# Optimization experiments

Measured on AMD Instinct MI355X. Metric: run time of the kernel, lower is better.

The kernel has to match this reference:

```python
import jax, jax.numpy as jnp
import numpy as np

SCALE = 1.0 / 16.0      # spatial scale: image coords -> feature-map coords (stride-16 backbone)
OUT = 7                 # roi_pool_outsize
RATIO = 2               # sampling_ratio
NUM_CLASSES = 21
HID = 1024
SCORE_THRESH = 0.05
NMS_THRESH = 0.5
DET = 100               # detections_per_img
MIN_SIZE = 0.01
LOG_MAX = float(np.log(1000.0 / 16.0))  # standard bbox decode dw/dh clamp


def _bilinear(feat, ys, xs):
    # feat [C,H,W]; ys [Py], xs [Px] -> [C,Py,Px] (torchvision roi_align interpolation, aligned=False)
    C, H, W = feat.shape
    vy = (ys > -1.0) & (ys < H)
    vx = (xs > -1.0) & (xs < W)
    y = jnp.clip(ys, 0.0, H - 1.0)
    x = jnp.clip(xs, 0.0, W - 1.0)
    y0 = jnp.floor(y).astype(jnp.int32)
    x0 = jnp.floor(x).astype(jnp.int32)
    y1 = jnp.minimum(y0 + 1, H - 1)
    x1 = jnp.minimum(x0 + 1, W - 1)
    ly = (y - y0)[:, None]
    lx = (x - x0)[None, :]
    f00 = feat[:, y0[:, None], x0[None, :]]
    f01 = feat[:, y0[:, None], x1[None, :]]
    f10 = feat[:, y1[:, None], x0[None, :]]
    f11 = feat[:, y1[:, None], x1[None, :]]
    val = (f00 * (1.0 - ly) * (1.0 - lx) + f01 * (1.0 - ly) * lx
           + f10 * ly * (1.0 - lx) + f11 * ly * lx)
    return val * (vy[:, None] & vx[None, :])


def _roi_align(features, boxes, bidx):
    # features [N,C,H,W], boxes [R,4] (image coords), bidx [R] -> [R,C,OUT,OUT]
    N, C, H, W = features.shape
    b = boxes * SCALE
    rw = jnp.maximum(b[:, 2] - b[:, 0], 1.0)
    rh = jnp.maximum(b[:, 3] - b[:, 1], 1.0)
    bw = rw / OUT
    bh = rh / OUT
    # per-bin sample offsets: (ph + (i+0.5)/ratio) for ph in [0,OUT), i in [0,RATIO)
    g = (jnp.arange(OUT, dtype=jnp.float32)[:, None]
         + (jnp.arange(RATIO, dtype=jnp.float32)[None, :] + 0.5) / RATIO).reshape(-1)  # [OUT*RATIO]
    ys = b[:, 1][:, None] + g[None, :] * bh[:, None]  # [R, OUT*RATIO]
    xs = b[:, 0][:, None] + g[None, :] * bw[:, None]
    vals = jax.vmap(lambda i, yr, xr: _bilinear(features[i], yr, xr))(bidx, ys, xs)  # [R,C,P,P]
    R = boxes.shape[0]
    return vals.reshape(R, C, OUT, RATIO, OUT, RATIO).mean(axis=(3, 5))


def _decode(deltas, props):
    # deltas [R,K,4], props [R,4]; weights (10,10,5,5) as in the module
    pw = props[:, 2] - props[:, 0]
    ph = props[:, 3] - props[:, 1]
    pcx = props[:, 0] + 0.5 * pw
    pcy = props[:, 1] + 0.5 * ph
    dx = deltas[..., 0] / 10.0
    dy = deltas[..., 1] / 10.0
    dw = jnp.minimum(deltas[..., 2] / 5.0, LOG_MAX)
    dh = jnp.minimum(deltas[..., 3] / 5.0, LOG_MAX)
    cx = dx * pw[:, None] + pcx[:, None]
    cy = dy * ph[:, None] + pcy[:, None]
    w = jnp.exp(dw) * pw[:, None]
    h = jnp.exp(dh) * ph[:, None]
    return jnp.stack([cx - 0.5 * w, cy - 0.5 * h, cx + 0.5 * w, cy + 0.5 * h], axis=-1)


def _per_image(scores, boxes, img):
    # scores [S,K], boxes [S,K,4]. Drop background class, flatten, filter, class-aware NMS, top-DET.
    S, K = scores.shape
    sc = scores[:, 1:].reshape(-1)                 # [M]
    bx = boxes[:, 1:, :].reshape(-1, 4)            # [M,4]
    lb = jnp.broadcast_to(jnp.arange(1, K, dtype=jnp.int32)[None, :], (S, K - 1)).reshape(-1)
    wv = bx[:, 2] - bx[:, 0]
    hv = bx[:, 3] - bx[:, 1]
    valid = (sc > SCORE_THRESH) & (wv >= MIN_SIZE) & (hv >= MIN_SIZE)
    live0 = jnp.where(valid, sc, -1.0)
    # batched_nms via per-class coordinate offsets
    nb = bx + (lb.astype(bx.dtype) * (img + 1.0))[:, None]
    areas = (nb[:, 2] - nb[:, 0]) * (nb[:, 3] - nb[:, 1])

    def step(live, _):
        i = jnp.argmax(live)
        s = live[i]
        b = nb[i]
        xx1 = jnp.maximum(b[0], nb[:, 0])
        yy1 = jnp.maximum(b[1], nb[:, 1])
        xx2 = jnp.minimum(b[2], nb[:, 2])
        yy2 = jnp.minimum(b[3], nb[:, 3])
        inter = jnp.maximum(xx2 - xx1, 0.0) * jnp.maximum(yy2 - yy1, 0.0)
        area_i = (b[2] - b[0]) * (b[3] - b[1])
        iou = inter / (area_i + areas - inter + 1e-9)
        live = jnp.where(iou > NMS_THRESH, -1.0, live)  # also suppresses i itself (iou=1)
        return live, (i, s)

    _, (idxs, svals) = jax.lax.scan(step, live0, None, length=DET)
    keep = svals > SCORE_THRESH
    out_boxes = jnp.where(keep[:, None], bx[idxs], 0.0)
    out_scores = jnp.where(keep, svals, 0.0)
    out_labels = jnp.where(keep, lb[idxs], 0)
    return out_boxes, out_scores, out_labels


def _forward(features, proposals, w1, b1, w2, b2, wc, bc, wb, bb, image_size):
    N, C, H, W = features.shape
    S = proposals.shape[1]
    props = proposals.reshape(-1, 4)
    bidx = jnp.repeat(jnp.arange(N), S)
    feats = _roi_align(features, props, bidx)          # [R,C,7,7]
    x = feats.reshape(N * S, -1)                       # [R, C*49]
    h = jax.nn.relu(x @ w1 + b1)
    h = jax.nn.relu(h @ w2 + b2)
    cls = h @ wc + bc                                  # [R,K]
    deltas = (h @ wb + bb).reshape(N * S, NUM_CLASSES, 4)
    scores = jax.nn.softmax(cls, axis=-1)
    boxes = _decode(deltas, props)                     # [R,K,4]
    img = float(image_size)
    boxes = jnp.clip(boxes, 0.0, img)                  # square image -> clip both coords to [0,img]
    scores = scores.reshape(N, S, NUM_CLASSES)
    boxes = boxes.reshape(N, S, NUM_CLASSES, 4)
    return jax.vmap(lambda s, bx: _per_image(s, bx, img))(scores, boxes)


def setup_inputs() -> dict:
    key = jax.random.key(0)
    ks = jax.random.split(key, 12)
    N, S, C, H, W = 2, 512, 512, 50, 50
    IMG = 800
    features = jax.random.normal(ks[0], (N, C, H, W), jnp.float32)
    x1 = jax.random.uniform(ks[1], (N, S)) * (IMG - 80.0)
    y1 = jax.random.uniform(ks[2], (N, S)) * (IMG - 80.0)
    x2 = jnp.minimum(x1 + 16.0 + jax.random.uniform(ks[3], (N, S)) * 180.0, float(IMG))
    y2 = jnp.minimum(y1 + 16.0 + jax.random.uniform(ks[4], (N, S)) * 180.0, float(IMG))
    proposals = jnp.stack([x1, y1, x2, y2], axis=-1)
    D = C * OUT * OUT  # 25088
    w1 = jax.random.normal(ks[5], (D, HID), jnp.float32) * 0.01
    b1 = jnp.zeros((HID,), jnp.float32)
    w2 = jax.random.normal(ks[6], (HID, HID), jnp.float32) * 0.02
    b2 = jnp.zeros((HID,), jnp.float32)
    wc = jax.random.normal(ks[7], (HID, NUM_CLASSES), jnp.float32) * 0.05
    bc = jnp.zeros((NUM_CLASSES,), jnp.float32)
    wb = jax.random.normal(ks[8], (HID, NUM_CLASSES * 4), jnp.float32) * 0.02
    bb = jnp.zeros((NUM_CLASSES * 4,), jnp.float32)
    return {"features": features, "proposals": proposals, "w1": w1, "b1": b1,
            "w2": w2, "b2": b2, "wc": wc, "bc": bc, "wb": wb, "bb": bb,
            "image_size": IMG}


def reference(features, proposals, w1, b1, w2, b2, wc, bc, wb, bb, image_size):
    boxes, scores, labels = _forward(features, proposals, w1, b1, w2, b2, wc, bc, wb, bb, image_size)
    return boxes, scores, labels
```

## Files before the change

### kernel.cpp

```cpp
#include <hip/hip_runtime.h>
#include <cmath>

#define NIMG 2
#define SPROP 512
#define NROI 1024
#define CCH 512
#define FH 50
#define FW 50
#define K1 25088
#define HID 1024
#define NCLS 21
#define NDET 100
#define IMGSZ 800.0f
#define LOGMAX 4.135166556742356f
#define MCAND 10240
#define ZSPLIT 8
#define KCHUNK 3136
#define ZSPLIT2 4
#define KCHUNK2 256

typedef unsigned short u16;
typedef __attribute__((ext_vector_type(8))) short short8;
typedef __attribute__((ext_vector_type(4))) float f32x4;
typedef __attribute__((ext_vector_type(16))) float f32x16;

__device__ __forceinline__ u16 f2bf(float x) {
  unsigned int u = __float_as_uint(x);
  u += 0x7fffu + ((u >> 16) & 1u);
  return (u16)(u >> 16);
}
__device__ __forceinline__ float bf2f(u16 h) {
  return __uint_as_float(((unsigned int)h) << 16);
}

template <bool BF16OUT>
__global__ __launch_bounds__(256) void roi_kernel(
    const float* __restrict__ feat, const float* __restrict__ props,
    float* __restrict__ X, u16* __restrict__ Xhi, u16* __restrict__ Xlo) {
  const int r = blockIdx.x;
  const int n = r >> 9;
  const int tid = threadIdx.x;
  __shared__ float tile[32][256];
  __shared__ int sy0[14], sy1[14], sx0[14], sx1[14];
  __shared__ float sly[14], slx[14], svy[14], svx[14];

  const float p0 = props[r * 4 + 0] * 0.0625f;
  const float p1 = props[r * 4 + 1] * 0.0625f;
  const float p2 = props[r * 4 + 2] * 0.0625f;
  const float p3 = props[r * 4 + 3] * 0.0625f;
  const float bw = fmaxf(p2 - p0, 1.0f) / 7.0f;
  const float bh = fmaxf(p3 - p1, 1.0f) / 7.0f;

  if (tid < 14) {
    const int j = tid;
    const float g = (float)(j >> 1) + ((float)(j & 1) + 0.5f) * 0.5f;
    float y = p1 + g * bh;
    svy[j] = (y > -1.0f && y < (float)FH) ? 1.0f : 0.0f;
    float yc = fminf(fmaxf(y, 0.0f), (float)(FH - 1));
    int y0 = (int)floorf(yc);
    sy0[j] = y0; sy1[j] = min(y0 + 1, FH - 1); sly[j] = yc - (float)y0;
    float x = p0 + g * bw;
    svx[j] = (x > -1.0f && x < (float)FW) ? 1.0f : 0.0f;
    float xc = fminf(fmaxf(x, 0.0f), (float)(FW - 1));
    int x0 = (int)floorf(xc);
    sx0[j] = x0; sx1[j] = min(x0 + 1, FW - 1); slx[j] = xc - (float)x0;
  }
  __syncthreads();
  const int ymin = sy0[0], xmin = sx0[0];
  const float* fb = feat + (size_t)n * CCH * (FH * FW);

  for (int cc = 0; cc < 16; ++cc) {
    const int c0 = cc * 32;
#pragma unroll
    for (int e = 0; e < 32; ++e) {
      const int idx = tid + e * 256;
      const int c = idx >> 8, p = idx & 255;
      const int gy = min(ymin + (p >> 4), FH - 1);
      const int gx = min(xmin + (p & 15), FW - 1);
      tile[c][p] = fb[(size_t)(c0 + c) * (FH * FW) + gy * FW + gx];
    }
    __syncthreads();
#pragma unroll
    for (int e = 0; e < 7; ++e) {
      const int idx = tid + e * 256;
      if (idx < 1568) {
        const int c = idx / 49;
        const int s = idx - c * 49;
        const int oy = s / 7, ox = s - (s / 7) * 7;
        float acc = 0.0f;
#pragma unroll
        for (int sy = 0; sy < 2; ++sy) {
          const int yj = oy * 2 + sy;
          const int py0 = sy0[yj] - ymin, py1 = sy1[yj] - ymin;
          const float ly = sly[yj], vy = svy[yj];
#pragma unroll
          for (int sx = 0; sx < 2; ++sx) {
            const int xj = ox * 2 + sx;
            const int px0 = sx0[xj] - xmin, px1 = sx1[xj] - xmin;
            const float lx = slx[xj], vx = svx[xj];
            const float f00 = tile[c][py0 * 16 + px0];
            const float f01 = tile[c][py0 * 16 + px1];
            const float f10 = tile[c][py1 * 16 + px0];
            const float f11 = tile[c][py1 * 16 + px1];
            float v = f00 * (1.0f - ly) * (1.0f - lx) + f01 * (1.0f - ly) * lx +
                      f10 * ly * (1.0f - lx) + f11 * ly * lx;
            acc += v * (vy * vx);
          }
        }
        const float v = acc * 0.25f;
        const size_t k = (size_t)r * K1 + (size_t)(c0 + c) * 49 + s;
        if (BF16OUT) {
          const u16 h = f2bf(v);
          Xhi[k] = h;
          Xlo[k] = f2bf(v - bf2f(h));
        } else {
          X[k] = v;
        }
      }
    }
    __syncthreads();
  }
}

template <int KDIM>
__global__ __launch_bounds__(256) void convw_kernel(
    const float* __restrict__ w, u16* __restrict__ Wh, u16* __restrict__ Wl) {
  __shared__ u16 sh[64][65], sl[64][65];
  const int k0 = blockIdx.x * 64;
  const int n0 = blockIdx.y * 64;
  const int t = threadIdx.x;
#pragma unroll
  for (int e = 0; e < 16; ++e) {
    const int idx = t + e * 256;
    const int kl = idx >> 6, nl = idx & 63;
    const float v = w[(size_t)(k0 + kl) * HID + n0 + nl];
    const u16 h = f2bf(v);
    sh[kl][nl] = h;
    sl[kl][nl] = f2bf(v - bf2f(h));
  }
  __syncthreads();
#pragma unroll
  for (int e = 0; e < 16; ++e) {
    const int idx = t + e * 256;
    const int nl = idx >> 6, kl = idx & 63;
    Wh[(size_t)(n0 + nl) * KDIM + k0 + kl] = sh[kl][nl];
    Wl[(size_t)(n0 + nl) * KDIM + k0 + kl] = sl[kl][nl];
  }
}

template <int KS, int KCH, bool SWZ>
__global__ __launch_bounds__(512, 4) void gemm_mfma_split(
    const u16* __restrict__ Ahg, const u16* __restrict__ Alg,
    const u16* __restrict__ Bhg, const u16* __restrict__ Blg,
    float* __restrict__ CP) {
  __shared__ u16 Ah[128][32], Al[128][32], Bh[128][32], Bl[128][32];
  const int tid = threadIdx.x;
  const int lane = tid & 63;
  const int wv = tid >> 6;
  const int wm = (wv >> 1) << 5;
  const int wn = (wv & 1) << 6;

  int bx = blockIdx.x, by = blockIdx.y, bz = blockIdx.z;
  if (SWZ) {
    const int f = blockIdx.x + ((blockIdx.y + (blockIdx.z << 3)) << 3);
    bz = f & 7;
    const int u = f >> 3;
    bx = u & 7;
    by = u >> 3;
  }
  const int mT = by << 7;
  const int nT = bx << 7;
  const int kz = bz * KCH;
  const int kend = kz + KCH;

  const int sr = tid >> 2;
  const int sq = (tid & 3) << 3;
  const int scw = (((tid & 3) ^ ((sr >> 1) & 3)) << 3);
  const size_t aoff = (size_t)(mT + sr) * KS;
  const size_t boff = (size_t)(nT + sr) * KS;

  f32x16 acc[2];
#pragma unroll
  for (int j = 0; j < 2; ++j)
#pragma unroll
    for (int e = 0; e < 16; ++e) acc[j][e] = 0.0f;

  const int fm = lane & 31;
  const int fh = lane >> 5;
  const int vswz = (fm >> 1) & 3;

  uint4 rA = *(const uint4*)(Ahg + aoff + kz + sq);
  uint4 rL = *(const uint4*)(Alg + aoff + kz + sq);
  uint4 rB = *(const uint4*)(Bhg + boff + kz + sq);
  uint4 rM = *(const uint4*)(Blg + boff + kz + sq);
  uint4 sA = *(const uint4*)(Ahg + aoff + kz + 32 + sq);
  uint4 sL = *(const uint4*)(Alg + aoff + kz + 32 + sq);
  uint4 sB = *(const uint4*)(Bhg + boff + kz + 32 + sq);
  uint4 sM = *(const uint4*)(Blg + boff + kz + 32 + sq);

  auto compute = [&]() {
#pragma unroll
    for (int kh = 0; kh < 2; ++kh) {
      const int cA = ((((kh << 1) | fh) ^ vswz) << 3);
      const short8 fah = *(const short8*)(&Ah[wm + fm][cA]);
      const short8 fal = *(const short8*)(&Al[wm + fm][cA]);
      short8 fbh[2], fbl[2];
      fbh[0] = *(const short8*)(&Bh[wn + fm][cA]);
      fbh[1] = *(const short8*)(&Bh[wn + 32 + fm][cA]);
      fbl[0] = *(const short8*)(&Bl[wn + fm][cA]);
      fbl[1] = *(const short8*)(&Bl[wn + 32 + fm][cA]);
#pragma unroll
      for (int tj = 0; tj < 2; ++tj) {
        acc[tj] = __builtin_amdgcn_mfma_f32_32x32x16_bf16(fah, fbh[tj], acc[tj], 0, 0, 0);
        acc[tj] = __builtin_amdgcn_mfma_f32_32x32x16_bf16(fah, fbl[tj], acc[tj], 0, 0, 0);
        acc[tj] = __builtin_amdgcn_mfma_f32_32x32x16_bf16(fal, fbh[tj], acc[tj], 0, 0, 0);
      }
    }
  };

  for (int kb = kz; kb < kend; kb += 64) {
    *(uint4*)(&Ah[sr][scw]) = rA;
    *(uint4*)(&Al[sr][scw]) = rL;
    *(uint4*)(&Bh[sr][scw]) = rB;
    *(uint4*)(&Bl[sr][scw]) = rM;
    __syncthreads();
    const int kn1 = (kb + 64 < kend) ? kb + 64 : kz;
    rA = *(const uint4*)(Ahg + aoff + kn1 + sq);
    rL = *(const uint4*)(Alg + aoff + kn1 + sq);
    rB = *(const uint4*)(Bhg + boff + kn1 + sq);
    rM = *(const uint4*)(Blg + boff + kn1 + sq);
    compute();
    __syncthreads();
    *(uint4*)(&Ah[sr][scw]) = sA;
    *(uint4*)(&Al[sr][scw]) = sL;
    *(uint4*)(&Bh[sr][scw]) = sB;
    *(uint4*)(&Bl[sr][scw]) = sM;
    __syncthreads();
    const int kn2 = (kb + 96 < kend) ? kb + 96 : kz;
    sA = *(const uint4*)(Ahg + aoff + kn2 + sq);
    sL = *(const uint4*)(Alg + aoff + kn2 + sq);
    sB = *(const uint4*)(Bhg + boff + kn2 + sq);
    sM = *(const uint4*)(Blg + boff + kn2 + sq);
    compute();
    __syncthreads();
  }

  float* Cp = CP + (size_t)bz * ((size_t)NROI * HID);
  const int ccol = nT + wn + fm;
  const int rbase = mT + wm + (fh << 2);
#pragma unroll
  for (int tj = 0; tj < 2; ++tj)
#pragma unroll
    for (int rg = 0; rg < 16; ++rg) {
      const int row = rbase + (rg & 3) + 8 * (rg >> 2);
      Cp[(size_t)row * HID + ccol + tj * 32] = acc[tj][rg];
    }
}

__global__ __launch_bounds__(256) void gemm1_kernel(
    const float* __restrict__ A, const float* __restrict__ B,
    float* __restrict__ CP) {
  __shared__ float As[16][68];
  __shared__ float Bs[16][68];
  const int tid = threadIdx.x;
  const int mTile = blockIdx.y << 6;
  const int nTile = blockIdx.x << 6;
  const int k0 = blockIdx.z * KCHUNK;
  const int ty = tid >> 4, tx = tid & 15;
  const int ar = tid >> 2, ac = (tid & 3) << 2;
  const int br = tid >> 4, bcl = (tid & 15) << 2;
  float acc[4][4] = {};

  for (int kb = k0; kb < k0 + KCHUNK; kb += 16) {
    const float4 av = *(const float4*)(A + (size_t)(mTile + ar) * K1 + kb + ac);
    const float4 bv = *(const float4*)(B + (size_t)(kb + br) * HID + nTile + bcl);
    As[ac + 0][ar] = av.x; As[ac + 1][ar] = av.y;
    As[ac + 2][ar] = av.z; As[ac + 3][ar] = av.w;
    *(float4*)(&Bs[br][bcl]) = bv;
    __syncthreads();
#pragma unroll
    for (int kk = 0; kk < 16; ++kk) {
      const float4 a4 = *(const float4*)(&As[kk][ty << 2]);
      const float4 b4 = *(const float4*)(&Bs[kk][tx << 2]);
      const float aa[4] = {a4.x, a4.y, a4.z, a4.w};
      const float bb4[4] = {b4.x, b4.y, b4.z, b4.w};
#pragma unroll
      for (int i = 0; i < 4; ++i)
#pragma unroll
        for (int j = 0; j < 4; ++j)
          acc[i][j] = fmaf(aa[i], bb4[j], acc[i][j]);
    }
    __syncthreads();
  }
  float* Cp = CP + (size_t)blockIdx.z * (HID * NROI);
#pragma unroll
  for (int i = 0; i < 4; ++i) {
    *(float4*)(Cp + (size_t)(mTile + (ty << 2) + i) * HID + nTile + (tx << 2)) =
        make_float4(acc[i][0], acc[i][1], acc[i][2], acc[i][3]);
  }
}

__global__ __launch_bounds__(256) void bias_relu_bf16_kernel(
    const float* __restrict__ CP, const float* __restrict__ b1,
    u16* __restrict__ H1h, u16* __restrict__ H1l) {
  const int idx = blockIdx.x * 256 + threadIdx.x;
  float v = b1[idx & (HID - 1)];
#pragma unroll
  for (int z = 0; z < ZSPLIT; ++z) v += CP[(size_t)z * (HID * NROI) + idx];
  v = fmaxf(v, 0.0f);
  const u16 h = f2bf(v);
  H1h[idx] = h;
  H1l[idx] = f2bf(v - bf2f(h));
}

__global__ __launch_bounds__(256) void bias_relu_f32_kernel(
    const float* __restrict__ CP, const float* __restrict__ b1,
    float* __restrict__ H1) {
  const int idx = blockIdx.x * 256 + threadIdx.x;
  float v = b1[idx & (HID - 1)];
#pragma unroll
  for (int z = 0; z < ZSPLIT; ++z) v += CP[(size_t)z * (HID * NROI) + idx];
  H1[idx] = fmaxf(v, 0.0f);
}

__global__ __launch_bounds__(256) void bias_relu2_kernel(
    const float* __restrict__ CP2, const float* __restrict__ b2,
    float* __restrict__ H2) {
  const int idx = blockIdx.x * 256 + threadIdx.x;
  float v = b2[idx & (HID - 1)];
#pragma unroll
  for (int z = 0; z < ZSPLIT2; ++z) v += CP2[(size_t)z * (HID * NROI) + idx];
  H2[idx] = fmaxf(v, 0.0f);
}

__global__ __launch_bounds__(256) void gemm2_kernel(
    const float* __restrict__ A, const float* __restrict__ B,
    const float* __restrict__ bias, float* __restrict__ C) {
  __shared__ float As[16][68];
  __shared__ float Bs[16][68];
  const int tid = threadIdx.x;
  const int mTile = blockIdx.y << 6;
  const int nTile = blockIdx.x << 6;
  const int ty = tid >> 4, tx = tid & 15;
  const int ar = tid >> 2, ac = (tid & 3) << 2;
  const int br = tid >> 4, bcl = (tid & 15) << 2;
  float acc[4][4] = {};

  for (int kb = 0; kb < HID; kb += 16) {
    const float4 av = *(const float4*)(A + (size_t)(mTile + ar) * HID + kb + ac);
    const float4 bv = *(const float4*)(B + (size_t)(kb + br) * HID + nTile + bcl);
    As[ac + 0][ar] = av.x; As[ac + 1][ar] = av.y;
    As[ac + 2][ar] = av.z; As[ac + 3][ar] = av.w;
    *(float4*)(&Bs[br][bcl]) = bv;
    __syncthreads();
#pragma unroll
    for (int kk = 0; kk < 16; ++kk) {
      const float4 a4 = *(const float4*)(&As[kk][ty << 2]);
      const float4 b4 = *(const float4*)(&Bs[kk][tx << 2]);
      const float aa[4] = {a4.x, a4.y, a4.z, a4.w};
      const float bb4[4] = {b4.x, b4.y, b4.z, b4.w};
#pragma unroll
      for (int i = 0; i < 4; ++i)
#pragma unroll
        for (int j = 0; j < 4; ++j)
          acc[i][j] = fmaf(aa[i], bb4[j], acc[i][j]);
    }
    __syncthreads();
  }
#pragma unroll
  for (int i = 0; i < 4; ++i) {
#pragma unroll
    for (int j = 0; j < 4; ++j) {
      float v = acc[i][j] + bias[nTile + (tx << 2) + j];
      acc[i][j] = fmaxf(v, 0.0f);
    }
    *(float4*)(C + (size_t)(mTile + (ty << 2) + i) * HID + nTile + (tx << 2)) =
        make_float4(acc[i][0], acc[i][1], acc[i][2], acc[i][3]);
  }
}

__global__ __launch_bounds__(128) void heads_kernel(
    const float* __restrict__ H2m, const float* __restrict__ wc,
    const float* __restrict__ bc, const float* __restrict__ wb,
    const float* __restrict__ bb, const float* __restrict__ props,
    float* __restrict__ BX2, float* __restrict__ NB2,
    float* __restrict__ LV2) {
  const int r = blockIdx.x;
  const int tid = threadIdx.x;
  __shared__ float hrow[HID];
  __shared__ float vals[112];
  __shared__ float red[2];

  for (int i = tid; i < HID; i += 128) hrow[i] = H2m[(size_t)r * HID + i];
  __syncthreads();

  if (tid < 105) {
    float acc;
    if (tid < NCLS) {
      acc = bc[tid];
      for (int kk = 0; kk < HID; ++kk) acc = fmaf(hrow[kk], wc[kk * NCLS + tid], acc);
    } else {
      const int j = tid - NCLS;
      acc = bb[j];
      for (int kk = 0; kk < HID; ++kk) acc = fmaf(hrow[kk], wb[kk * (NCLS * 4) + j], acc);
    }
    vals[tid] = acc;
  }
  __syncthreads();

  if (tid == 0) {
    float m = vals[0];
    for (int k = 1; k < NCLS; ++k) m = fmaxf(m, vals[k]);
    float s = 0.0f;
    for (int k = 0; k < NCLS; ++k) s += expf(vals[k] - m);
    red[0] = m;
    red[1] = 1.0f / s;
  }
  __syncthreads();

  if (tid >= 1 && tid <= 20) {
    const int k = tid;
    const float prob = expf(vals[k] - red[0]) * red[1];

    const float px1 = props[r * 4 + 0], py1 = props[r * 4 + 1];
    const float px2 = props[r * 4 + 2], py2 = props[r * 4 + 3];
    const float pw = px2 - px1, ph = py2 - py1;
    const float pcx = px1 + 0.5f * pw, pcy = py1 + 0.5f * ph;

    const float dx = vals[NCLS + k * 4 + 0] / 10.0f;
    const float dy = vals[NCLS + k * 4 + 1] / 10.0f;
    const float dw = fminf(vals[NCLS + k * 4 + 2] / 5.0f, LOGMAX);
    const float dh = fminf(vals[NCLS + k * 4 + 3] / 5.0f, LOGMAX);

    const float cx = dx * pw + pcx, cy = dy * ph + pcy;
    const float w = expf(dw) * pw, h = expf(dh) * ph;
    float b0 = cx - 0.5f * w, b1c = cy - 0.5f * h;
    float b2 = cx + 0.5f * w, b3 = cy + 0.5f * h;
    b0 = fminf(fmaxf(b0, 0.0f), IMGSZ);
    b1c = fminf(fmaxf(b1c, 0.0f), IMGSZ);
    b2 = fminf(fmaxf(b2, 0.0f), IMGSZ);
    b3 = fminf(fmaxf(b3, 0.0f), IMGSZ);

    const float wv = b2 - b0, hv = b3 - b1c;
    const bool valid = (prob > 0.05f) && (wv >= 0.01f) && (hv >= 0.01f);

    const int n = r >> 9, s = r & 511;
    const int cand = (k - 1) * SPROP + s;
    const size_t bi = (size_t)n * MCAND + cand;
    const float off = (float)k * (IMGSZ + 1.0f);

    BX2[bi * 4 + 0] = b0; BX2[bi * 4 + 1] = b1c;
    BX2[bi * 4 + 2] = b2; BX2[bi * 4 + 3] = b3;
    NB2[bi * 4 + 0] = b0 + off; NB2[bi * 4 + 1] = b1c + off;
    NB2[bi * 4 + 2] = b2 + off; NB2[bi * 4 + 3] = b3 + off;
    LV2[bi] = valid ? prob : -1.0f;
  }
}

template <int CTRL>
__device__ __forceinline__ void red2(float& v, int& ix) {
  const float tv = __int_as_float(__builtin_amdgcn_update_dpp(
      (int)0xC0000000, __float_as_int(v), CTRL, 0xf, 0xf, false));
  const int ti = __builtin_amdgcn_update_dpp(0x7fffffff, ix, CTRL, 0xf, 0xf, false);
  if (tv > v || (tv == v && ti < ix)) { v = tv; ix = ti; }
}
__device__ __forceinline__ void wave_red2(float& v, int& ix) {
  red2<0x111>(v, ix);
  red2<0x112>(v, ix);
  red2<0x114>(v, ix);
  red2<0x118>(v, ix);
  red2<0x142>(v, ix);
  red2<0x143>(v, ix);
}

__global__ __launch_bounds__(64) void nms_class_kernel(
    const float* __restrict__ NB2, const float* __restrict__ LV2,
    float* __restrict__ ksg, int* __restrict__ kig, int* __restrict__ cntg) {
  const int bid = blockIdx.x;
  const int lane = threadIdx.x;
  __shared__ float4 lbox[SPROP];
  const size_t cb = (size_t)bid * SPROP;

  float lv[8], b0[8], b1[8], b2[8], b3[8], ar[8];
#pragma unroll
  for (int j = 0; j < 8; ++j) {
    const int s = lane + j * 64;
    lv[j] = LV2[cb + s];
    const float4 b = *(const float4*)(NB2 + (cb + s) * 4);
    b0[j] = b.x; b1[j] = b.y; b2[j] = b.z; b3[j] = b.w;
    ar[j] = (b.z - b.x) * (b.w - b.y);
    lbox[s] = b;
  }

  int cnt = 0;
  for (int d = 0; d < NDET; ++d) {
    float bv = -2.0f;
    int bix = 0x7fffffff;
#pragma unroll
    for (int j = 0; j < 8; ++j) {
      if (lv[j] > bv) { bv = lv[j]; bix = lane + j * 64; }
    }
    wave_red2(bv, bix);
    const float bv2 = __shfl(bv, 63);
    const int bix2 = __shfl(bix, 63);
    if (bv2 <= 0.05f) break;

    if (lane == 0) {
      ksg[bid * NDET + cnt] = bv2;
      kig[bid * NDET + cnt] = bix2;
    }
    ++cnt;

    const float4 wb = lbox[bix2];
    const float wa = (wb.z - wb.x) * (wb.w - wb.y);
#pragma unroll
    for (int j = 0; j < 8; ++j) {
      const float xx1 = fmaxf(wb.x, b0[j]);
      const float yy1 = fmaxf(wb.y, b1[j]);
      const float xx2 = fminf(wb.z, b2[j]);
      const float yy2 = fminf(wb.w, b3[j]);
      const float inter = fmaxf(xx2 - xx1, 0.0f) * fmaxf(yy2 - yy1, 0.0f);
      const float iou = inter / (wa + ar[j] - inter + 1e-9f);
      if (iou > 0.5f) lv[j] = -1.0f;
    }
  }
  if (lane == 0) cntg[bid] = cnt;
}

__global__ __launch_bounds__(1024) void nms_merge_kernel(
    const float* __restrict__ ksg, const int* __restrict__ kig,
    const int* __restrict__ cntg, const float* __restrict__ BX2,
    float* __restrict__ out) {
  const int n = blockIdx.x;
  const int tid = threadIdx.x;
  __shared__ int cbase[21];
  __shared__ unsigned long long keys[2000];
  __shared__ float ssc[2000];
  __shared__ int sfl[2000];
  __shared__ float svals[NDET];
  __shared__ int sflat[NDET];

  if (tid == 0) {
    int acc = 0;
    for (int c = 0; c < 20; ++c) { cbase[c] = acc; acc += cntg[n * 20 + c]; }
    cbase[20] = acc;
  }
  __syncthreads();
  const int T = cbase[20];

  for (int idx = tid; idx < 20 * NDET; idx += 1024) {
    const int c = idx / NDET, e = idx - (idx / NDET) * NDET;
    if (e < cntg[n * 20 + c]) {
      const int pos = cbase[c] + e;
      const float s = ksg[(n * 20 + c) * NDET + e];
      const int slot = kig[(n * 20 + c) * NDET + e];
      const int flat = slot * 20 + c;
      ssc[pos] = s;
      sfl[pos] = flat;
      keys[pos] = ((unsigned long long)__float_as_uint(s) << 32) |
                  (unsigned long long)(0xFFFFFFFFu - (unsigned)flat);
    }
  }
  __syncthreads();

  float msc[2]; int mfl[2]; unsigned long long mk[2]; int rank[2] = {0, 0};
  bool own[2];
#pragma unroll
  for (int e = 0; e < 2; ++e) {
    const int i = tid + e * 1024;
    own[e] = (i < T);
    if (own[e]) { mk[e] = keys[i]; msc[e] = ssc[i]; mfl[e] = sfl[i]; }
  }
  for (int i = 0; i < T; ++i) {
    const unsigned long long k = keys[i];
    if (own[0] && k > mk[0]) ++rank[0];
    if (own[1] && k > mk[1]) ++rank[1];
  }
#pragma unroll
  for (int e = 0; e < 2; ++e)
    if (own[e] && rank[e] < NDET) { svals[rank[e]] = msc[e]; sflat[rank[e]] = mfl[e]; }
  __syncthreads();

  if (tid < NDET) {
    const int m = (T < NDET) ? T : NDET;
    const bool keep = tid < m;
    float sv = 0.0f;
    float4 bx4 = make_float4(0.0f, 0.0f, 0.0f, 0.0f);
    float label = 0.0f;
    if (keep) {
      sv = svals[tid];
      const int flat = sflat[tid];
      const int c = flat % 20, s = flat / 20;
      bx4 = *(const float4*)(BX2 + ((size_t)(n * 20 + c) * SPROP + s) * 4);
      label = (float)(c + 1);
    }
    out[(n * NDET + tid) * 4 + 0] = bx4.x;
    out[(n * NDET + tid) * 4 + 1] = bx4.y;
    out[(n * NDET + tid) * 4 + 2] = bx4.z;
    out[(n * NDET + tid) * 4 + 3] = bx4.w;
    out[NIMG * NDET * 4 + n * NDET + tid] = sv;
    out[NIMG * NDET * 4 + NIMG * NDET + n * NDET + tid] = label;
  }
}

extern "C" void kernel_launch(void* const* d_in, const int* in_sizes, int n_in,
                              void* d_out, int out_size, void* d_ws, size_t ws_size,
                              hipStream_t stream) {
  const float* features  = (const float*)d_in[0];
  const float* proposals = (const float*)d_in[1];
  const float* w1 = (const float*)d_in[2];
  const float* b1 = (const float*)d_in[3];
  const float* w2 = (const float*)d_in[4];
  const float* b2 = (const float*)d_in[5];
  const float* wc = (const float*)d_in[6];
  const float* bc = (const float*)d_in[7];
  const float* wb = (const float*)d_in[8];
  const float* bb = (const float*)d_in[9];

  const size_t XE = (size_t)NROI * K1;
  const size_t WE = (size_t)K1 * HID;
  const size_t FLOATS_TAIL =
      (size_t)ZSPLIT * NROI * HID + 2 * (size_t)NROI * HID + (size_t)NIMG * MCAND * 10;
  const size_t NEED = (XE * 2 + WE * 2) * sizeof(u16) + FLOATS_TAIL * sizeof(float);

  if (ws_size >= NEED) {
    u16* Xhi = (u16*)d_ws;
    u16* Xlo = Xhi + XE;
    u16* Wh  = Xlo + XE;
    u16* Wl  = Wh + WE;
    float* CP  = (float*)(Wl + WE);
    float* CP2 = CP;
    float* H2  = CP + (size_t)ZSPLIT * NROI * HID;
    float* BX2 = H2 + (size_t)NROI * HID;
    float* NB2 = BX2 + (size_t)NIMG * MCAND * 4;
    float* LV2 = NB2 + (size_t)NIMG * MCAND * 4;
    float* ksg = LV2 + (size_t)NIMG * MCAND;
    int*   kig = (int*)(ksg + (size_t)NIMG * 20 * NDET);
    int*   cntg = kig + (size_t)NIMG * 20 * NDET;
    u16* H1h = Xhi;
    u16* H1l = Xhi + (size_t)NROI * HID;
    u16* W2h = Xlo;
    u16* W2l = Xlo + (size_t)HID * HID;

    convw_kernel<K1><<<dim3(K1 / 64, HID / 64), 256, 0, stream>>>(w1, Wh, Wl);
    roi_kernel<true><<<NROI, 256, 0, stream>>>(features, proposals, nullptr, Xhi, Xlo);
    gemm_mfma_split<K1, KCHUNK, true><<<dim3(8, 8, ZSPLIT), 512, 0, stream>>>(
        Xhi, Xlo, Wh, Wl, CP);
    bias_relu_bf16_kernel<<<(NROI * HID) / 256, 256, 0, stream>>>(CP, b1, H1h, H1l);
    convw_kernel<HID><<<dim3(HID / 64, HID / 64), 256, 0, stream>>>(w2, W2h, W2l);
    gemm_mfma_split<HID, KCHUNK2, false><<<dim3(8, 8, ZSPLIT2), 512, 0, stream>>>(
        H1h, H1l, W2h, W2l, CP2);
    bias_relu2_kernel<<<(NROI * HID) / 256, 256, 0, stream>>>(CP2, b2, H2);
    heads_kernel<<<NROI, 128, 0, stream>>>(H2, wc, bc, wb, bb, proposals,
                                           BX2, NB2, LV2);
    nms_class_kernel<<<NIMG * 20, 64, 0, stream>>>(NB2, LV2, ksg, kig, cntg);
    nms_merge_kernel<<<NIMG, 1024, 0, stream>>>(ksg, kig, cntg, BX2,
                                                (float*)d_out);
  } else {
    float* ws = (float*)d_ws;
    float* X   = ws;
    float* CP  = X + XE;
    float* H1  = CP + (size_t)ZSPLIT * NROI * HID;
    float* H2  = H1 + (size_t)NROI * HID;
    float* BX2 = H2 + (size_t)NROI * HID;
    float* NB2 = BX2 + (size_t)NIMG * MCAND * 4;
    float* LV2 = NB2 + (size_t)NIMG * MCAND * 4;
    float* ksg = LV2 + (size_t)NIMG * MCAND;
    int*   kig = (int*)(ksg + (size_t)NIMG * 20 * NDET);
    int*   cntg = kig + (size_t)NIMG * 20 * NDET;

    roi_kernel<false><<<NROI, 256, 0, stream>>>(features, proposals, X, nullptr, nullptr);
    gemm1_kernel<<<dim3(16, 16, ZSPLIT), 256, 0, stream>>>(X, w1, CP);
    bias_relu_f32_kernel<<<(NROI * HID) / 256, 256, 0, stream>>>(CP, b1, H1);
    gemm2_kernel<<<dim3(16, 16), 256, 0, stream>>>(H1, w2, b2, H2);
    heads_kernel<<<NROI, 128, 0, stream>>>(H2, wc, bc, wb, bb, proposals,
                                           BX2, NB2, LV2);
    nms_class_kernel<<<NIMG * 20, 64, 0, stream>>>(NB2, LV2, ksg, kig, cntg);
    nms_merge_kernel<<<NIMG, 1024, 0, stream>>>(ksg, kig, cntg, BX2,
                                                (float*)d_out);
  }
}
```

Measured before the change: 840.6 us.

## Widen split-K MFMA GEMM tile to 128x256 with 64x64 per-wave subtiles

```diff
diff --git a/kernel.cpp b/kernel.cpp
--- a/kernel.cpp
+++ b/kernel.cpp
@@ -16,8 +16,8 @@
 #define MCAND 10240
 #define ZSPLIT 8
 #define KCHUNK 3136
-#define ZSPLIT2 4
-#define KCHUNK2 256
+#define ZSPLIT2 8
+#define KCHUNK2 128
 
 typedef unsigned short u16;
 typedef __attribute__((ext_vector_type(8))) short short8;
@@ -149,98 +149,119 @@
 }
 
 template <int KS, int KCH, bool SWZ>
-__global__ __launch_bounds__(512, 4) void gemm_mfma_split(
+__global__ __launch_bounds__(512, 2) void gemm_mfma_split(
     const u16* __restrict__ Ahg, const u16* __restrict__ Alg,
     const u16* __restrict__ Bhg, const u16* __restrict__ Blg,
     float* __restrict__ CP) {
-  __shared__ u16 Ah[128][32], Al[128][32], Bh[128][32], Bl[128][32];
+  __shared__ u16 Ah[128][32], Al[128][32], Bh[256][32], Bl[256][32];
   const int tid = threadIdx.x;
   const int lane = tid & 63;
   const int wv = tid >> 6;
-  const int wm = (wv >> 1) << 5;
-  const int wn = (wv & 1) << 6;
+  const int wm = (wv >> 2) << 6;
+  const int wn = (wv & 3) << 6;
 
   int bx = blockIdx.x, by = blockIdx.y, bz = blockIdx.z;
   if (SWZ) {
-    const int f = blockIdx.x + ((blockIdx.y + (blockIdx.z << 3)) << 3);
+    const int f = blockIdx.x + ((blockIdx.y + (blockIdx.z << 3)) << 2);
     bz = f & 7;
     const int u = f >> 3;
-    bx = u & 7;
-    by = u >> 3;
+    bx = u & 3;
+    by = u >> 2;
   }
   const int mT = by << 7;
-  const int nT = bx << 7;
+  const int nT = bx << 8;
   const int kz = bz * KCH;
   const int kend = kz + KCH;
 
   const int sr = tid >> 2;
   const int sq = (tid & 3) << 3;
   const int scw = (((tid & 3) ^ ((sr >> 1) & 3)) << 3);
-  const size_t aoff = (size_t)(mT + sr) * KS;
-  const size_t boff = (size_t)(nT + sr) * KS;
-
-  f32x16 acc[2];
-#pragma unroll
-  for (int j = 0; j < 2; ++j)
-#pragma unroll
-    for (int e = 0; e < 16; ++e) acc[j][e] = 0.0f;
+  const size_t aoff  = (size_t)(mT + sr) * KS + sq;
+  const size_t b0off = (size_t)(nT + sr) * KS + sq;
+  const size_t b1off = (size_t)(nT + sr + 128) * KS + sq;
+
+  f32x16 acc[2][2];
+#pragma unroll
+  for (int i = 0; i < 2; ++i)
+#pragma unroll
+    for (int j = 0; j < 2; ++j)
+#pragma unroll
+      for (int e = 0; e < 16; ++e) acc[i][j][e] = 0.0f;
 
   const int fm = lane & 31;
   const int fh = lane >> 5;
   const int vswz = (fm >> 1) & 3;
 
-  uint4 rA = *(const uint4*)(Ahg + aoff + kz + sq);
-  uint4 rL = *(const uint4*)(Alg + aoff + kz + sq);
-  uint4 rB = *(const uint4*)(Bhg + boff + kz + sq);
-  uint4 rM = *(const uint4*)(Blg + boff + kz + sq);
-  uint4 sA = *(const uint4*)(Ahg + aoff + kz + 32 + sq);
-  uint4 sL = *(const uint4*)(Alg + aoff + kz + 32 + sq);
-  uint4 sB = *(const uint4*)(Bhg + boff + kz + 32 + sq);
-  uint4 sM = *(const uint4*)(Blg + boff + kz + 32 + sq);
+  uint4 rA  = *(const uint4*)(Ahg + aoff + kz);
+  uint4 rL  = *(const uint4*)(Alg + aoff + kz);
+  uint4 rB0 = *(const uint4*)(Bhg + b0off + kz);
+  uint4 rB1 = *(const uint4*)(Bhg + b1off + kz);
+  uint4 rM0 = *(const uint4*)(Blg + b0off + kz);
+  uint4 rM1 = *(const uint4*)(Blg + b1off + kz);
+  uint4 sA  = *(const uint4*)(Ahg + aoff + kz + 32);
+  uint4 sL  = *(const uint4*)(Alg + aoff + kz + 32);
+  uint4 sB0 = *(const uint4*)(Bhg + b0off + kz + 32);
+  uint4 sB1 = *(const uint4*)(Bhg + b1off + kz + 32);
+  uint4 sM0 = *(const uint4*)(Blg + b0off + kz + 32);
+  uint4 sM1 = *(const uint4*)(Blg + b1off + kz + 32);
 
   auto compute = [&]() {
 #pragma unroll
     for (int kh = 0; kh < 2; ++kh) {
       const int cA = ((((kh << 1) | fh) ^ vswz) << 3);
-      const short8 fah = *(const short8*)(&Ah[wm + fm][cA]);
-      const short8 fal = *(const short8*)(&Al[wm + fm][cA]);
-      short8 fbh[2], fbl[2];
-      fbh[0] = *(const short8*)(&Bh[wn + fm][cA]);
-      fbh[1] = *(const short8*)(&Bh[wn + 32 + fm][cA]);
-      fbl[0] = *(const short8*)(&Bl[wn + fm][cA]);
-      fbl[1] = *(const short8*)(&Bl[wn + 32 + fm][cA]);
-#pragma unroll
-      for (int tj = 0; tj < 2; ++tj) {
-        acc[tj] = __builtin_amdgcn_mfma_f32_32x32x16_bf16(fah, fbh[tj], acc[tj], 0, 0, 0);
-        acc[tj] = __builtin_amdgcn_mfma_f32_32x32x16_bf16(fah, fbl[tj], acc[tj], 0, 0, 0);
-        acc[tj] = __builtin_amdgcn_mfma_f32_32x32x16_bf16(fal, fbh[tj], acc[tj], 0, 0, 0);
+      short8 fa_h[2], fa_l[2], fb_h[2], fb_l[2];
+#pragma unroll
+      for (int t = 0; t < 2; ++t) {
+        fa_h[t] = *(const short8*)(&Ah[wm + t * 32 + fm][cA]);
+        fa_l[t] = *(const short8*)(&Al[wm + t * 32 + fm][cA]);
+        fb_h[t] = *(const short8*)(&Bh[wn + t * 32 + fm][cA]);
+        fb_l[t] = *(const short8*)(&Bl[wn + t * 32 + fm][cA]);
       }
+#pragma unroll
+      for (int ti = 0; ti < 2; ++ti)
+#pragma unroll
+        for (int tj = 0; tj < 2; ++tj) {
+          acc[ti][tj] = __builtin_amdgcn_mfma_f32_32x32x16_bf16(
+              fa_h[ti], fb_h[tj], acc[ti][tj], 0, 0, 0);
+          acc[ti][tj] = __builtin_amdgcn_mfma_f32_32x32x16_bf16(
+              fa_h[ti], fb_l[tj], acc[ti][tj], 0, 0, 0);
+          acc[ti][tj] = __builtin_amdgcn_mfma_f32_32x32x16_bf16(
+              fa_l[ti], fb_h[tj], acc[ti][tj], 0, 0, 0);
+        }
     }
   };
 
   for (int kb = kz; kb < kend; kb += 64) {
     *(uint4*)(&Ah[sr][scw]) = rA;
     *(uint4*)(&Al[sr][scw]) = rL;
-    *(uint4*)(&Bh[sr][scw]) = rB;
-    *(uint4*)(&Bl[sr][scw]) = rM;
+    *(uint4*)(&Bh[sr][scw]) = rB0;
+    *(uint4*)(&Bh[sr + 128][scw]) = rB1;
+    *(uint4*)(&Bl[sr][scw]) = rM0;
+    *(uint4*)(&Bl[sr + 128][scw]) = rM1;
     __syncthreads();
     const int kn1 = (kb + 64 < kend) ? kb + 64 : kz;
-    rA = *(const uint4*)(Ahg + aoff + kn1 + sq);
-    rL = *(const uint4*)(Alg + aoff + kn1 + sq);
-    rB = *(const uint4*)(Bhg + boff + kn1 + sq);
-    rM = *(const uint4*)(Blg + boff + kn1 + sq);
+    rA  = *(const uint4*)(Ahg + aoff + kn1);
+    rL  = *(const uint4*)(Alg + aoff + kn1);
+    rB0 = *(const uint4*)(Bhg + b0off + kn1);
+    rB1 = *(const uint4*)(Bhg + b1off + kn1);
+    rM0 = *(const uint4*)(Blg + b0off + kn1);
+    rM1 = *(const uint4*)(Blg + b1off + kn1);
     compute();
     __syncthreads();
     *(uint4*)(&Ah[sr][scw]) = sA;
     *(uint4*)(&Al[sr][scw]) = sL;
-    *(uint4*)(&Bh[sr][scw]) = sB;
-    *(uint4*)(&Bl[sr][scw]) = sM;
+    *(uint4*)(&Bh[sr][scw]) = sB0;
+    *(uint4*)(&Bh[sr + 128][scw]) = sB1;
+    *(uint4*)(&Bl[sr][scw]) = sM0;
+    *(uint4*)(&Bl[sr + 128][scw]) = sM1;
     __syncthreads();
     const int kn2 = (kb + 96 < kend) ? kb + 96 : kz;
-    sA = *(const uint4*)(Ahg + aoff + kn2 + sq);
-    sL = *(const uint4*)(Alg + aoff + kn2 + sq);
-    sB = *(const uint4*)(Bhg + boff + kn2 + sq);
-    sM = *(const uint4*)(Blg + boff + kn2 + sq);
+    sA  = *(const uint4*)(Ahg + aoff + kn2);
+    sL  = *(const uint4*)(Alg + aoff + kn2);
+    sB0 = *(const uint4*)(Bhg + b0off + kn2);
+    sB1 = *(const uint4*)(Bhg + b1off + kn2);
+    sM0 = *(const uint4*)(Blg + b0off + kn2);
+    sM1 = *(const uint4*)(Blg + b1off + kn2);
     compute();
     __syncthreads();
   }
@@ -249,12 +270,14 @@
   const int ccol = nT + wn + fm;
   const int rbase = mT + wm + (fh << 2);
 #pragma unroll
-  for (int tj = 0; tj < 2; ++tj)
-#pragma unroll
-    for (int rg = 0; rg < 16; ++rg) {
-      const int row = rbase + (rg & 3) + 8 * (rg >> 2);
-      Cp[(size_t)row * HID + ccol + tj * 32] = acc[tj][rg];
-    }
+  for (int ti = 0; ti < 2; ++ti)
+#pragma unroll
+    for (int tj = 0; tj < 2; ++tj)
+#pragma unroll
+      for (int rg = 0; rg < 16; ++rg) {
+        const int row = rbase + ti * 32 + (rg & 3) + 8 * (rg >> 2);
+        Cp[(size_t)row * HID + ccol + tj * 32] = acc[ti][tj][rg];
+      }
 }
 
 __global__ __launch_bounds__(256) void gemm1_kernel(
@@ -644,11 +667,11 @@
 
     convw_kernel<K1><<<dim3(K1 / 64, HID / 64), 256, 0, stream>>>(w1, Wh, Wl);
     roi_kernel<true><<<NROI, 256, 0, stream>>>(features, proposals, nullptr, Xhi, Xlo);
-    gemm_mfma_split<K1, KCHUNK, true><<<dim3(8, 8, ZSPLIT), 512, 0, stream>>>(
+    gemm_mfma_split<K1, KCHUNK, true><<<dim3(4, 8, ZSPLIT), 512, 0, stream>>>(
         Xhi, Xlo, Wh, Wl, CP);
     bias_relu_bf16_kernel<<<(NROI * HID) / 256, 256, 0, stream>>>(CP, b1, H1h, H1l);
     convw_kernel<HID><<<dim3(HID / 64, HID / 64), 256, 0, stream>>>(w2, W2h, W2l);
-    gemm_mfma_split<HID, KCHUNK2, false><<<dim3(8, 8, ZSPLIT2), 512, 0, stream>>>(
+    gemm_mfma_split<HID, KCHUNK2, true><<<dim3(4, 8, ZSPLIT2), 512, 0, stream>>>(
         H1h, H1l, W2h, W2l, CP2);
     bias_relu2_kernel<<<(NROI * HID) / 256, 256, 0, stream>>>(CP2, b2, H2);
     heads_kernel<<<NROI, 128, 0, stream>>>(H2, wc, bc, wb, bb, proposals,
```

Measured after the change: 835.4 us. No clear change (-0.6%).
